# Optimization experiments

Hardware: AMD Instinct MI355X
Metric: run time of the kernel (lower is better)

Reference implementation:

```python
import jax, jax.numpy as jnp
import numpy as np

N, D, B, H = 131072, 512, 512, 8  # nodes, hidden_dim, graphs, heads


def setup_inputs() -> dict:
    key = jax.random.key(0)
    ks = jax.random.split(key, 4)
    x = jax.random.normal(ks[0], (N, D), jnp.float32)
    # sorted segment ids; every graph nonempty (matches torch batch.max()+1 semantics)
    batch = jnp.sort(jnp.arange(N, dtype=jnp.int32) % B)
    query = jax.random.normal(ks[1], (D,), jnp.float32)          # nn.Parameter(randn(1,1,D))
    W_in = jax.random.normal(ks[2], (3 * D, D), jnp.float32) / np.sqrt(D)  # MHA in_proj_weight
    b_in = jnp.zeros((3 * D,), jnp.float32)
    W_out = jax.random.normal(ks[3], (D, D), jnp.float32) / np.sqrt(D)     # MHA out_proj
    b_out = jnp.zeros((D,), jnp.float32)
    return {"x": x, "batch": batch, "num_graphs": B, "query": query,
            "W_in": W_in, "b_in": b_in, "W_out": W_out, "b_out": b_out}


def reference(x, batch, num_graphs, query, W_in, b_in, W_out, b_out):
    # Fused ragged single-query multihead attention pooling (eval mode: dropout off).
    D = x.shape[1]
    dh = D // H
    scale = 1.0 / np.sqrt(dh)
    # q/k/v projections (torch MHA packed in_proj: rows [0:D]=q, [D:2D]=k, [2D:3D]=v)
    q = ((query @ W_in[:D].T + b_in[:D]) * scale).reshape(H, dh)       # [H, dh], shared across graphs
    k = (x @ W_in[D:2 * D].T + b_in[D:2 * D]).reshape(-1, H, dh)       # [N, H, dh]
    v = (x @ W_in[2 * D:].T + b_in[2 * D:]).reshape(-1, H, dh)         # [N, H, dh]
    scores = jnp.einsum('nhd,hd->nh', k, q)                             # [N, H]
    # segment (per-graph) softmax over nodes
    smax = jax.ops.segment_max(scores, batch, num_segments=num_graphs)  # [B, H]
    e = jnp.exp(scores - smax[batch])
    denom = jax.ops.segment_sum(e, batch, num_segments=num_graphs)      # [B, H]
    p = e / denom[batch]                                                # [N, H]
    pooled = jax.ops.segment_sum(p[:, :, None] * v, batch, num_segments=num_graphs)  # [B, H, dh]
    return pooled.reshape(num_graphs, D) @ W_out.T + b_out              # [B, D]
```

## Files before the change

### kernel.cpp

```cpp
#include <hip/hip_runtime.h>
#include <math.h>

#define NHEAD 8

template <int CTRL>
__device__ __forceinline__ float dpp_add(float v) {
    int r = __builtin_amdgcn_mov_dpp(__float_as_int(v), CTRL, 0xF, 0xF, false);
    return v + __int_as_float(r);
}

__device__ __forceinline__ float swap16_add(float v) {
    int a = __float_as_int(v);
    int b;
    asm volatile("v_mov_b32 %1, %0\n\t"
                 "s_nop 1\n\t"
                 "v_permlane16_swap_b32 %0, %1\n\t"
                 "s_nop 1"
                 : "+v"(a), "=&v"(b));
    return __int_as_float(a) + __int_as_float(b);
}
__device__ __forceinline__ float swap32_add(float v) {
    int a = __float_as_int(v);
    int b;
    asm volatile("v_mov_b32 %1, %0\n\t"
                 "s_nop 1\n\t"
                 "v_permlane32_swap_b32 %0, %1\n\t"
                 "s_nop 1"
                 : "+v"(a), "=&v"(b));
    return __int_as_float(a) + __int_as_float(b);
}

__device__ __forceinline__ float wave_allsum(float v) {
    v = dpp_add<0xB1>(v);
    v = dpp_add<0x4E>(v);
    v = dpp_add<0x141>(v);
    v = dpp_add<0x140>(v);
    v = swap16_add(v);
    v = swap32_add(v);
    return v;
}

__global__ void __launch_bounds__(256) k_setup(const float* __restrict__ query,
                                               const float* __restrict__ W_in,
                                               const float* __restrict__ b_in,
                                               const int* __restrict__ batch,
                                               float* __restrict__ wsc,
                                               int* __restrict__ seg_start,
                                               int* __restrict__ seg_end,
                                               int N, float scale) {
    const int g = blockIdx.x, t = threadIdx.x;
    if (g < 16) {
        __shared__ float qs4[64][4];
        __shared__ float qs[64];
        const int h = g >> 1, half = g & 1;
        {
            const int d = t & 63, qtr = t >> 6;
            const int row = h * 64 + d;
            const float4* wq = reinterpret_cast<const float4*>(W_in + (size_t)row * 512 + qtr * 128);
            const float4* qv = reinterpret_cast<const float4*>(query + qtr * 128);
            float a = 0.f;
#pragma unroll 8
            for (int i = 0; i < 32; ++i) {
                float4 w = wq[i], q = qv[i];
                a += w.x * q.x + w.y * q.y + w.z * q.z + w.w * q.w;
            }
            qs4[d][qtr] = a;
        }
        __syncthreads();
        if (t < 64) {
            const float s = qs4[t][0] + qs4[t][1] + qs4[t][2] + qs4[t][3];
            qs[t] = (s + b_in[h * 64 + t]) * scale;
        }
        __syncthreads();
        const int i = half * 256 + t;
        const float* Wk = W_in + (size_t)512 * 512;
        float a = 0.f;
#pragma unroll 8
        for (int d = 0; d < 64; ++d)
            a += qs[d] * Wk[(size_t)(h * 64 + d) * 512 + i];
        wsc[h * 512 + i] = a;
    } else {
        const int stride = (gridDim.x - 16) * 256;
        for (int n = (g - 16) * 256 + t; n < N; n += stride) {
            int b = batch[n];
            if (n == 0 || batch[n - 1] != b) seg_start[b] = n;
            if (n == N - 1 || batch[n + 1] != b) seg_end[b] = n + 1;
        }
    }
}

__global__ void __launch_bounds__(256, 2) k_fused1(const float* __restrict__ x,
                                                   const float* __restrict__ wsc,
                                                   const int* __restrict__ seg_start,
                                                   const int* __restrict__ seg_end,
                                                   float* __restrict__ xp) {
    __shared__ float mrg[4][64][64];
    __shared__ float dsum[4][NHEAD];
    const int b = blockIdx.x, t = threadIdx.x;
    const int lane = t & 63, w = t >> 6;
    const int s0 = seg_start[b], s1 = seg_end[b];
    const int len = s1 - s0;
    const int clen = (len + 3) >> 2;
    const int r0 = s0 + w * clen;
    const int r1 = min(s1, r0 + clen);

    float4 w0[NHEAD], w1[NHEAD];
#pragma unroll
    for (int h = 0; h < NHEAD; ++h) {
        w0[h] = *reinterpret_cast<const float4*>(wsc + h * 512 + lane * 8);
        w1[h] = *reinterpret_cast<const float4*>(wsc + h * 512 + lane * 8 + 4);
    }

    float acc[NHEAD][8];
#pragma unroll
    for (int h = 0; h < NHEAD; ++h)
#pragma unroll
        for (int j = 0; j < 8; ++j) acc[h][j] = 0.f;
    float dacc[NHEAD];
#pragma unroll
    for (int h = 0; h < NHEAD; ++h) dacc[h] = 0.f;

    const float* xl = x + lane * 8;
#define LD0(r) (*reinterpret_cast<const float4*>(xl + (size_t)(r) * 512))
#define LD1(r) (*reinterpret_cast<const float4*>(xl + (size_t)(r) * 512 + 4))

    float4 cA0, cA1, cB0, cB1, nA0, nA1, nB0, nB1, mA0, mA1, mB0, mB1;
    if (r0 + 0 < r1) { cA0 = LD0(r0 + 0); cA1 = LD1(r0 + 0); }
    if (r0 + 1 < r1) { cB0 = LD0(r0 + 1); cB1 = LD1(r0 + 1); }
    if (r0 + 2 < r1) { nA0 = LD0(r0 + 2); nA1 = LD1(r0 + 2); }
    if (r0 + 3 < r1) { nB0 = LD0(r0 + 3); nB1 = LD1(r0 + 3); }
    if (r0 + 4 < r1) { mA0 = LD0(r0 + 4); mA1 = LD1(r0 + 4); }
    if (r0 + 5 < r1) { mB0 = LD0(r0 + 5); mB1 = LD1(r0 + 5); }

    for (int r = r0; r < r1; r += 2) {
        const float4 a0 = cA0, a1 = cA1, b0 = cB0, b1 = cB1;
        cA0 = nA0; cA1 = nA1; cB0 = nB0; cB1 = nB1;
        nA0 = mA0; nA1 = mA1; nB0 = mB0; nB1 = mB1;
        if (r + 6 < r1) { mA0 = LD0(r + 6); mA1 = LD1(r + 6); }
        if (r + 7 < r1) { mB0 = LD0(r + 7); mB1 = LD1(r + 7); }

        const bool hasB = (r + 1 < r1);
        float eA[NHEAD], eB[NHEAD];
#pragma unroll
        for (int h = 0; h < NHEAD; ++h) {
            float dA = a0.x * w0[h].x + a0.y * w0[h].y + a0.z * w0[h].z + a0.w * w0[h].w +
                       a1.x * w1[h].x + a1.y * w1[h].y + a1.z * w1[h].z + a1.w * w1[h].w;
            float dB = b0.x * w0[h].x + b0.y * w0[h].y + b0.z * w0[h].z + b0.w * w0[h].w +
                       b1.x * w1[h].x + b1.y * w1[h].y + b1.z * w1[h].z + b1.w * w1[h].w;
            eA[h] = __expf(wave_allsum(dA));
            eB[h] = __expf(wave_allsum(dB));
        }
#pragma unroll
        for (int h = 0; h < NHEAD; ++h) {
            dacc[h] += eA[h];
            acc[h][0] += eA[h] * a0.x; acc[h][1] += eA[h] * a0.y;
            acc[h][2] += eA[h] * a0.z; acc[h][3] += eA[h] * a0.w;
            acc[h][4] += eA[h] * a1.x; acc[h][5] += eA[h] * a1.y;
            acc[h][6] += eA[h] * a1.z; acc[h][7] += eA[h] * a1.w;
        }
        if (hasB) {
#pragma unroll
            for (int h = 0; h < NHEAD; ++h) {
                dacc[h] += eB[h];
                acc[h][0] += eB[h] * b0.x; acc[h][1] += eB[h] * b0.y;
                acc[h][2] += eB[h] * b0.z; acc[h][3] += eB[h] * b0.w;
                acc[h][4] += eB[h] * b1.x; acc[h][5] += eB[h] * b1.y;
                acc[h][6] += eB[h] * b1.z; acc[h][7] += eB[h] * b1.w;
            }
        }
    }
#undef LD0
#undef LD1

#pragma unroll
    for (int h = 0; h < NHEAD; ++h)
#pragma unroll
        for (int j = 0; j < 8; ++j)
            mrg[w][h * 8 + j][lane] = acc[h][j];
    if (lane == 0) {
#pragma unroll
        for (int h = 0; h < NHEAD; ++h) dsum[w][h] = dacc[h];
    }
    __syncthreads();

    {
        const int c0i = 2 * t;
        const int lsrc = c0i >> 3, slot = c0i & 7;
        float* xpb = xp + (size_t)b * (NHEAD * 512);
#pragma unroll
        for (int h = 0; h < NHEAD; ++h) {
            const float den = dsum[0][h] + dsum[1][h] + dsum[2][h] + dsum[3][h];
            const float rl = 1.f / den;
            float num0 = 0.f, num1 = 0.f;
#pragma unroll
            for (int g = 0; g < 4; ++g) {
                num0 += mrg[g][h * 8 + slot][lsrc];
                num1 += mrg[g][h * 8 + slot + 1][lsrc];
            }
            float2 o;
            o.x = num0 * rl;
            o.y = num1 * rl;
            *reinterpret_cast<float2*>(xpb + (size_t)h * 512 + c0i) = o;
        }
    }
}

__global__ void __launch_bounds__(256) k_gemm_tn4w(const float* __restrict__ A, int lda, int zA,
                                                   const float* __restrict__ Bm, int ldb, int zB,
                                                   const float* __restrict__ bias, int zBias,
                                                   float* __restrict__ C, int ldc, int zC, int K) {
    __shared__ float As[4][32][36];
    __shared__ float Bs[4][32][36];
    __shared__ float red[4][32][32];
    const int z = blockIdx.z;
    A += (size_t)z * zA;
    Bm += (size_t)z * zB;
    bias += (size_t)z * zBias;
    C += (size_t)z * zC;
    const int m0 = blockIdx.x * 32, n0 = blockIdx.y * 32;
    const int t = threadIdx.x;
    const int w = t >> 6, lane = t & 63;
    const int row = lane >> 1, c0 = (lane & 1) * 16;
    const int ty = lane >> 3, tx = lane & 7;
    const int Kw = K >> 2;
    const int kw0 = w * Kw;
    float c[4][4];
#pragma unroll
    for (int i = 0; i < 4; ++i)
#pragma unroll
        for (int j = 0; j < 4; ++j) c[i][j] = 0.f;

    for (int kt = 0; kt < Kw; kt += 32) {
        const int k0 = kw0 + kt;
        const float* Ar = A + (size_t)(m0 + row) * lda + k0 + c0;
        const float* Br = Bm + (size_t)(n0 + row) * ldb + k0 + c0;
        float4 a4[4], b4[4];
#pragma unroll
        for (int j = 0; j < 4; ++j) {
            a4[j] = *reinterpret_cast<const float4*>(Ar + j * 4);
            b4[j] = *reinterpret_cast<const float4*>(Br + j * 4);
        }
#pragma unroll
        for (int j = 0; j < 4; ++j) {
            As[w][c0 + j * 4 + 0][row] = a4[j].x;
            As[w][c0 + j * 4 + 1][row] = a4[j].y;
            As[w][c0 + j * 4 + 2][row] = a4[j].z;
            As[w][c0 + j * 4 + 3][row] = a4[j].w;
            Bs[w][c0 + j * 4 + 0][row] = b4[j].x;
            Bs[w][c0 + j * 4 + 1][row] = b4[j].y;
            Bs[w][c0 + j * 4 + 2][row] = b4[j].z;
            Bs[w][c0 + j * 4 + 3][row] = b4[j].w;
        }
#pragma unroll
        for (int kk = 0; kk < 32; ++kk) {
            float4 av = *reinterpret_cast<const float4*>(&As[w][kk][ty * 4]);
            float4 bv = *reinterpret_cast<const float4*>(&Bs[w][kk][tx * 4]);
            c[0][0] += av.x * bv.x; c[0][1] += av.x * bv.y; c[0][2] += av.x * bv.z; c[0][3] += av.x * bv.w;
            c[1][0] += av.y * bv.x; c[1][1] += av.y * bv.y; c[1][2] += av.y * bv.z; c[1][3] += av.y * bv.w;
            c[2][0] += av.z * bv.x; c[2][1] += av.z * bv.y; c[2][2] += av.z * bv.z; c[2][3] += av.z * bv.w;
            c[3][0] += av.w * bv.x; c[3][1] += av.w * bv.y; c[3][2] += av.w * bv.z; c[3][3] += av.w * bv.w;
        }
    }
#pragma unroll
    for (int i = 0; i < 4; ++i)
#pragma unroll
        for (int j = 0; j < 4; ++j) red[w][ty * 4 + i][tx * 4 + j] = c[i][j];
    __syncthreads();
    const int r = t >> 3, cc = (t & 7) * 4;
    float4 s = {0.f, 0.f, 0.f, 0.f};
#pragma unroll
    for (int g = 0; g < 4; ++g) {
        const float4 v = *reinterpret_cast<const float4*>(&red[g][r][cc]);
        s.x += v.x; s.y += v.y; s.z += v.z; s.w += v.w;
    }
    const float4 bv4 = *reinterpret_cast<const float4*>(bias + n0 + cc);
    float4 o = {s.x + bv4.x, s.y + bv4.y, s.z + bv4.z, s.w + bv4.w};
    *reinterpret_cast<float4*>(C + (size_t)(m0 + r) * ldc + n0 + cc) = o;
}

extern "C" void kernel_launch(void* const* d_in, const int* in_sizes, int n_in,
                              void* d_out, int out_size, void* d_ws, size_t ws_size,
                              hipStream_t stream) {
    const float* x     = (const float*)d_in[0];
    const int*   batch = (const int*)d_in[1];
    const float* query = (const float*)d_in[3];
    const float* W_in  = (const float*)d_in[4];
    const float* b_in  = (const float*)d_in[5];
    const float* W_out = (const float*)d_in[6];
    const float* b_out = (const float*)d_in[7];
    float* out = (float*)d_out;

    const int D = in_sizes[3];
    const int N = in_sizes[0] / D;
    const int B = out_size / D;
    const int dh = D / NHEAD;
    const float scale = 1.0f / sqrtf((float)dh);

    float* wsf       = (float*)d_ws;
    float* wsc       = wsf;
    float* xp        = wsc + NHEAD * 512;
    float* pooled    = xp + (size_t)B * NHEAD * 512;
    int*   seg_start = (int*)(pooled + (size_t)B * 512);
    int*   seg_end   = seg_start + B;

    k_setup<<<16 + 256, 256, 0, stream>>>(query, W_in, b_in, batch, wsc,
                                          seg_start, seg_end, N, scale);

    k_fused1<<<B, 256, 0, stream>>>(x, wsc, seg_start, seg_end, xp);

    k_gemm_tn4w<<<dim3(B / 32, dh / 32, NHEAD), 256, 0, stream>>>(
        xp, NHEAD * 512, 512,
        W_in + (size_t)2 * D * D, D, dh * D,
        b_in + 2 * D, dh,
        pooled, D, dh, D);

    k_gemm_tn4w<<<dim3(B / 32, D / 32, 1), 256, 0, stream>>>(
        pooled, D, 0,
        W_out, D, 0,
        b_out, 0,
        out, D, 0, D);
}
```

Before: 109.4 us.

## Split segments across chunk blocks with fp16 dot scoring and a merge kernel

Each graph segment is now split across nc blocks (3 when workspace allows). Each block writes partial numerators and denominators, and a new merge kernel sums them and normalizes. Score dot products now use packed fp16 fdot2 on rtz-converted x and weights, and the LDS merge buffer is halved and processed in two passes. Launch bounds rise to 3 blocks per CU to raise occupancy and parallelism. In exchange it adds an extra kernel launch, extra partial-buffer traffic, and reduced precision in the attention scores (no max subtraction, so there is some overflow risk).

After: 110.2 us. No clear change (+0.7%).

```diff
diff --git a/kernel.cpp b/kernel.cpp
--- a/kernel.cpp
+++ b/kernel.cpp
@@ -2,6 +2,8 @@
 #include <math.h>
 
 #define NHEAD 8
+
+typedef __fp16 half2v __attribute__((ext_vector_type(2)));
 
 template <int CTRL>
 __device__ __forceinline__ float dpp_add(float v) {
@@ -89,26 +91,35 @@
     }
 }
 
-__global__ void __launch_bounds__(256, 2) k_fused1(const float* __restrict__ x,
+__global__ void __launch_bounds__(256, 3) k_fused1(const float* __restrict__ x,
                                                    const float* __restrict__ wsc,
                                                    const int* __restrict__ seg_start,
                                                    const int* __restrict__ seg_end,
-                                                   float* __restrict__ xp) {
-    __shared__ float mrg[4][64][64];
+                                                   float* __restrict__ xp_part,
+                                                   float* __restrict__ denom_part,
+                                                   int nc) {
+    __shared__ float mrg[4][32][64];
     __shared__ float dsum[4][NHEAD];
-    const int b = blockIdx.x, t = threadIdx.x;
+    const int b = blockIdx.x, c = blockIdx.y, t = threadIdx.x;
     const int lane = t & 63, w = t >> 6;
     const int s0 = seg_start[b], s1 = seg_end[b];
     const int len = s1 - s0;
-    const int clen = (len + 3) >> 2;
-    const int r0 = s0 + w * clen;
-    const int r1 = min(s1, r0 + clen);
-
-    float4 w0[NHEAD], w1[NHEAD];
+    const int clen = (len + nc - 1) / nc;
+    const int c0r = s0 + c * clen;
+    const int c1r = min(s1, c0r + clen);
+    const int wlen = (c1r - c0r + 3) >> 2;
+    const int r0 = c0r + w * wlen;
+    const int r1 = min(c1r, r0 + wlen);
+
+    half2v wh[NHEAD][4];
 #pragma unroll
     for (int h = 0; h < NHEAD; ++h) {
-        w0[h] = *reinterpret_cast<const float4*>(wsc + h * 512 + lane * 8);
-        w1[h] = *reinterpret_cast<const float4*>(wsc + h * 512 + lane * 8 + 4);
+        const float4 wa = *reinterpret_cast<const float4*>(wsc + h * 512 + lane * 8);
+        const float4 wb = *reinterpret_cast<const float4*>(wsc + h * 512 + lane * 8 + 4);
+        wh[h][0] = __builtin_amdgcn_cvt_pkrtz(wa.x, wa.y);
+        wh[h][1] = __builtin_amdgcn_cvt_pkrtz(wa.z, wa.w);
+        wh[h][2] = __builtin_amdgcn_cvt_pkrtz(wb.x, wb.y);
+        wh[h][3] = __builtin_amdgcn_cvt_pkrtz(wb.z, wb.w);
     }
 
     float acc[NHEAD][8];
@@ -124,84 +135,118 @@
 #define LD0(r) (*reinterpret_cast<const float4*>(xl + (size_t)(r) * 512))
 #define LD1(r) (*reinterpret_cast<const float4*>(xl + (size_t)(r) * 512 + 4))
 
-    float4 cA0, cA1, cB0, cB1, nA0, nA1, nB0, nB1, mA0, mA1, mB0, mB1;
-    if (r0 + 0 < r1) { cA0 = LD0(r0 + 0); cA1 = LD1(r0 + 0); }
-    if (r0 + 1 < r1) { cB0 = LD0(r0 + 1); cB1 = LD1(r0 + 1); }
-    if (r0 + 2 < r1) { nA0 = LD0(r0 + 2); nA1 = LD1(r0 + 2); }
-    if (r0 + 3 < r1) { nB0 = LD0(r0 + 3); nB1 = LD1(r0 + 3); }
-    if (r0 + 4 < r1) { mA0 = LD0(r0 + 4); mA1 = LD1(r0 + 4); }
-    if (r0 + 5 < r1) { mB0 = LD0(r0 + 5); mB1 = LD1(r0 + 5); }
-
-    for (int r = r0; r < r1; r += 2) {
-        const float4 a0 = cA0, a1 = cA1, b0 = cB0, b1 = cB1;
-        cA0 = nA0; cA1 = nA1; cB0 = nB0; cB1 = nB1;
-        nA0 = mA0; nA1 = mA1; nB0 = mB0; nB1 = mB1;
-        if (r + 6 < r1) { mA0 = LD0(r + 6); mA1 = LD1(r + 6); }
-        if (r + 7 < r1) { mB0 = LD0(r + 7); mB1 = LD1(r + 7); }
-
-        const bool hasB = (r + 1 < r1);
-        float eA[NHEAD], eB[NHEAD];
+    float4 a0, a1, n0, n1;
+    if (r0 + 0 < r1) { a0 = LD0(r0 + 0); a1 = LD1(r0 + 0); }
+    if (r0 + 1 < r1) { n0 = LD0(r0 + 1); n1 = LD1(r0 + 1); }
+
+    for (int r = r0; r < r1; ++r) {
+        const float4 c0 = a0, c1 = a1;
+        a0 = n0; a1 = n1;
+        if (r + 2 < r1) { n0 = LD0(r + 2); n1 = LD1(r + 2); }
+
+        const half2v xh0 = __builtin_amdgcn_cvt_pkrtz(c0.x, c0.y);
+        const half2v xh1 = __builtin_amdgcn_cvt_pkrtz(c0.z, c0.w);
+        const half2v xh2 = __builtin_amdgcn_cvt_pkrtz(c1.x, c1.y);
+        const half2v xh3 = __builtin_amdgcn_cvt_pkrtz(c1.z, c1.w);
+
+        float e[NHEAD];
 #pragma unroll
         for (int h = 0; h < NHEAD; ++h) {
-            float dA = a0.x * w0[h].x + a0.y * w0[h].y + a0.z * w0[h].z + a0.w * w0[h].w +
-                       a1.x * w1[h].x + a1.y * w1[h].y + a1.z * w1[h].z + a1.w * w1[h].w;
-            float dB = b0.x * w0[h].x + b0.y * w0[h].y + b0.z * w0[h].z + b0.w * w0[h].w +
-                       b1.x * w1[h].x + b1.y * w1[h].y + b1.z * w1[h].z + b1.w * w1[h].w;
-            eA[h] = __expf(wave_allsum(dA));
-            eB[h] = __expf(wave_allsum(dB));
+            float d = __builtin_amdgcn_fdot2(xh0, wh[h][0], 0.f, false);
+            d = __builtin_amdgcn_fdot2(xh1, wh[h][1], d, false);
+            d = __builtin_amdgcn_fdot2(xh2, wh[h][2], d, false);
+            d = __builtin_amdgcn_fdot2(xh3, wh[h][3], d, false);
+            e[h] = __expf(wave_allsum(d));
         }
 #pragma unroll
         for (int h = 0; h < NHEAD; ++h) {
-            dacc[h] += eA[h];
-            acc[h][0] += eA[h] * a0.x; acc[h][1] += eA[h] * a0.y;
-            acc[h][2] += eA[h] * a0.z; acc[h][3] += eA[h] * a0.w;
-            acc[h][4] += eA[h] * a1.x; acc[h][5] += eA[h] * a1.y;
-            acc[h][6] += eA[h] * a1.z; acc[h][7] += eA[h] * a1.w;
-        }
-        if (hasB) {
-#pragma unroll
-            for (int h = 0; h < NHEAD; ++h) {
-                dacc[h] += eB[h];
-                acc[h][0] += eB[h] * b0.x; acc[h][1] += eB[h] * b0.y;
-                acc[h][2] += eB[h] * b0.z; acc[h][3] += eB[h] * b0.w;
-                acc[h][4] += eB[h] * b1.x; acc[h][5] += eB[h] * b1.y;
-                acc[h][6] += eB[h] * b1.z; acc[h][7] += eB[h] * b1.w;
-            }
+            dacc[h] += e[h];
+            acc[h][0] += e[h] * c0.x; acc[h][1] += e[h] * c0.y;
+            acc[h][2] += e[h] * c0.z; acc[h][3] += e[h] * c0.w;
+            acc[h][4] += e[h] * c1.x; acc[h][5] += e[h] * c1.y;
+            acc[h][6] += e[h] * c1.z; acc[h][7] += e[h] * c1.w;
         }
     }
 #undef LD0
 #undef LD1
 
-#pragma unroll
-    for (int h = 0; h < NHEAD; ++h)
+    float* pb = xp_part + (size_t)(b * nc + c) * (NHEAD * 512);
+    if (lane == 0) {
+#pragma unroll
+        for (int h = 0; h < NHEAD; ++h) dsum[w][h] = dacc[h];
+    }
+#pragma unroll
+    for (int h = 0; h < 4; ++h)
 #pragma unroll
         for (int j = 0; j < 8; ++j)
             mrg[w][h * 8 + j][lane] = acc[h][j];
-    if (lane == 0) {
-#pragma unroll
-        for (int h = 0; h < NHEAD; ++h) dsum[w][h] = dacc[h];
-    }
-    __syncthreads();
-
+    __syncthreads();
     {
         const int c0i = 2 * t;
         const int lsrc = c0i >> 3, slot = c0i & 7;
-        float* xpb = xp + (size_t)b * (NHEAD * 512);
-#pragma unroll
-        for (int h = 0; h < NHEAD; ++h) {
-            const float den = dsum[0][h] + dsum[1][h] + dsum[2][h] + dsum[3][h];
-            const float rl = 1.f / den;
+#pragma unroll
+        for (int h = 0; h < 4; ++h) {
             float num0 = 0.f, num1 = 0.f;
 #pragma unroll
             for (int g = 0; g < 4; ++g) {
                 num0 += mrg[g][h * 8 + slot][lsrc];
                 num1 += mrg[g][h * 8 + slot + 1][lsrc];
             }
-            float2 o;
-            o.x = num0 * rl;
-            o.y = num1 * rl;
-            *reinterpret_cast<float2*>(xpb + (size_t)h * 512 + c0i) = o;
-        }
+            float2 o = {num0, num1};
+            *reinterpret_cast<float2*>(pb + (size_t)h * 512 + c0i) = o;
+        }
+    }
+    __syncthreads();
+#pragma unroll
+    for (int h = 4; h < NHEAD; ++h)
+#pragma unroll
+        for (int j = 0; j < 8; ++j)
+            mrg[w][(h - 4) * 8 + j][lane] = acc[h][j];
+    __syncthreads();
+    {
+        const int c0i = 2 * t;
+        const int lsrc = c0i >> 3, slot = c0i & 7;
+#pragma unroll
+        for (int h = 4; h < NHEAD; ++h) {
+            float num0 = 0.f, num1 = 0.f;
+#pragma unroll
+            for (int g = 0; g < 4; ++g) {
+                num0 += mrg[g][(h - 4) * 8 + slot][lsrc];
+                num1 += mrg[g][(h - 4) * 8 + slot + 1][lsrc];
+            }
+            float2 o = {num0, num1};
+            *reinterpret_cast<float2*>(pb + (size_t)h * 512 + c0i) = o;
+        }
+    }
+    if (t < NHEAD)
+        denom_part[(b * nc + c) * NHEAD + t] = dsum[0][t] + dsum[1][t] + dsum[2][t] + dsum[3][t];
+}
+
+__global__ void __launch_bounds__(256) k_merge(const float* __restrict__ xp_part,
+                                               const float* __restrict__ denom_part,
+                                               float* __restrict__ xp, int nc) {
+    const int b = blockIdx.x, t = threadIdx.x;
+    __shared__ float rd[NHEAD];
+    if (t < NHEAD) {
+        float d = 0.f;
+        for (int c = 0; c < nc; ++c) d += denom_part[(b * nc + c) * NHEAD + t];
+        rd[t] = 1.f / d;
+    }
+    __syncthreads();
+    const float2* src = reinterpret_cast<const float2*>(xp_part + (size_t)b * nc * NHEAD * 512);
+    float2* dst = reinterpret_cast<float2*>(xp + (size_t)b * NHEAD * 512);
+#pragma unroll
+    for (int i = 0; i < 8; ++i) {
+        const int idx = i * 256 + t;
+        const int h = idx >> 8;
+        float2 s = src[idx];
+        for (int c = 1; c < nc; ++c) {
+            const float2 v = src[(size_t)c * NHEAD * 256 + idx];
+            s.x += v.x; s.y += v.y;
+        }
+        const float r = rd[h];
+        s.x *= r; s.y *= r;
+        dst[idx] = s;
     }
 }
 
@@ -300,13 +345,27 @@
     float* wsc       = wsf;
     float* xp        = wsc + NHEAD * 512;
     float* pooled    = xp + (size_t)B * NHEAD * 512;
-    int*   seg_start = (int*)(pooled + (size_t)B * 512);
+    float* denom_ws  = pooled + (size_t)B * 512;
+    int*   seg_start = (int*)(denom_ws + (size_t)B * 4 * NHEAD);
     int*   seg_end   = seg_start + B;
+    float* tail      = (float*)(seg_end + B);
+
+    const size_t usedFloats = (size_t)(tail - wsf);
+    const size_t avail = ws_size / 4 - usedFloats;
+    int nc = 1;
+    float* xp_part = xp;
+    if (avail >= (size_t)B * 3 * NHEAD * 512) {
+        nc = 3;
+        xp_part = tail;
+    }
 
     k_setup<<<16 + 256, 256, 0, stream>>>(query, W_in, b_in, batch, wsc,
                                           seg_start, seg_end, N, scale);
 
-    k_fused1<<<B, 256, 0, stream>>>(x, wsc, seg_start, seg_end, xp);
+    k_fused1<<<dim3(B, nc), 256, 0, stream>>>(x, wsc, seg_start, seg_end,
+                                              xp_part, denom_ws, nc);
+
+    k_merge<<<B, 256, 0, stream>>>(xp_part, denom_ws, xp, nc);
 
     k_gemm_tn4w<<<dim3(B / 32, dh / 32, NHEAD), 256, 0, stream>>>(
         xp, NHEAD * 512, 512,
```
